# Performance work log

Hardware: AMD Instinct MI355X
Metric: run time of the kernel (lower is better)

## Reference

```python
import jax, jax.numpy as jnp
import numpy as np

K = 9  # 3x3 kernel taps

def conv2d(x, w, b):
    # stride 1, padding 1, NCHW / OIHW
    out = jax.lax.conv_general_dilated(x, w, (1, 1), ((1, 1), (1, 1)),
                                       dimension_numbers=('NCHW', 'OIHW', 'NCHW'))
    return out + b[None, :, None, None]

def deform_conv2d(x, offset, mask, w, b):
    # torchvision modulated deformable conv, kernel 3x3, stride 1, pad 1, dilation 1
    B, C, H, W = x.shape
    off = offset.reshape(B, K, 2, H, W)  # per-tap (dy, dx)
    ii = (jnp.arange(K) // 3).astype(x.dtype) - 1.0  # kernel row offset (pad=1)
    jj = (jnp.arange(K) % 3).astype(x.dtype) - 1.0   # kernel col offset
    hh = jnp.arange(H, dtype=x.dtype)[None, None, :, None]
    ww = jnp.arange(W, dtype=x.dtype)[None, None, None, :]
    py = hh + ii[None, :, None, None] + off[:, :, 0]  # [B,K,H,W] sample rows
    px = ww + jj[None, :, None, None] + off[:, :, 1]  # [B,K,H,W] sample cols

    y0 = jnp.floor(py); x0 = jnp.floor(px)
    dy = py - y0; dx = px - x0
    y0 = y0.astype(jnp.int32); x0 = x0.astype(jnp.int32)

    xf = x.reshape(B, C, H * W)

    def gather(yi, xi):
        valid = ((yi >= 0) & (yi < H) & (xi >= 0) & (xi < W)).astype(x.dtype)
        yc = jnp.clip(yi, 0, H - 1)
        xc = jnp.clip(xi, 0, W - 1)
        idx = (yc * W + xc).reshape(B, K * H * W)
        v = jax.vmap(lambda xb, ib: xb[:, ib])(xf, idx)  # [B,C,K*H*W]
        return v.reshape(B, C, K, H, W) * valid[:, None]

    v00 = gather(y0,     x0)
    v01 = gather(y0,     x0 + 1)
    v10 = gather(y0 + 1, x0)
    v11 = gather(y0 + 1, x0 + 1)

    dy = dy[:, None]; dx = dx[:, None]  # broadcast over channel dim
    val = (v00 * (1 - dy) * (1 - dx) + v01 * (1 - dy) * dx
           + v10 * dy * (1 - dx) + v11 * dy * dx)
    val = val * mask[:, None]  # sigmoid modulation, [B,1,K,H,W]

    out = jnp.einsum('ock,bckhw->bohw', w.reshape(w.shape[0], C, K), val)
    return out + b[None, :, None, None]

def setup_inputs() -> dict:
    key = jax.random.key(0)
    k1, k2, k3 = jax.random.split(key, 3)
    x = jax.random.normal(k1, (8, 3, 512, 512), dtype=jnp.float32)
    w_off = jax.random.normal(k2, (27, 3, 3, 3), dtype=jnp.float32) * 0.05
    b_off = jnp.zeros((27,), dtype=jnp.float32)
    w_def = jax.random.normal(k3, (3, 3, 3, 3), dtype=jnp.float32) * 0.1
    b_def = jnp.zeros((3,), dtype=jnp.float32)
    return {'x': x, 'w_off': w_off, 'b_off': b_off, 'w_def': w_def, 'b_def': b_def}

def reference(x, w_off, b_off, w_def, b_def):
    ow = conv2d(x, w_off, b_off)            # [B,27,H,W]
    offset = ow[:, :18]                      # 2*9 offsets
    mask = jax.nn.sigmoid(ow[:, 18:])        # 9 modulation masks
    return deform_conv2d(x, offset, mask, w_def, b_def)
```

## Files before the change

### kernel.cpp

```cpp
#include <hip/hip_runtime.h>
#include <math.h>

typedef float f2 __attribute__((ext_vector_type(2)));
typedef float f2u __attribute__((ext_vector_type(2), aligned(4)));
typedef float f4 __attribute__((ext_vector_type(4)));

#define BN 8
#define CIN 3
#define HH 512
#define WW 512
#define KK 9
#define PATCH 27
#define TAPBLK 96

__global__ void reorder_weights(const float* __restrict__ w_off,
                                const float* __restrict__ w_def,
                                float* __restrict__ ws)
{
    for (int idx = threadIdx.x; idx < KK * TAPBLK; idx += blockDim.x) {
        const int k = idx / TAPBLK;
        const int r = idx % TAPBLK;
        float v = 0.0f;
        if (r < 56) {
            const int q = r >> 1, half = r & 1;
            if (q < PATCH) v = w_off[(2 * k + half) * PATCH + q];
        } else if (r < 84) {
            const int i = r - 56;
            if (i < PATCH) v = w_off[(18 + k) * PATCH + i];
        } else {
            const int j = r - 84;
            const int c = j >> 2, o = j & 3;
            if (o < 3) v = w_def[o * PATCH + c * KK + k];
        }
        ws[idx] = v;
    }
}

__global__ __launch_bounds__(256) void deform_fused_kernel(
    const float* __restrict__ x,
    const float* __restrict__ wsw,
    const float* __restrict__ b_off,
    const float* __restrict__ b_def,
    float* __restrict__ out)
{
    const int w = blockIdx.x * blockDim.x + threadIdx.x;
    const int h = blockIdx.y;
    const int b = blockIdx.z;

    const size_t plane = (size_t)HH * WW;
    const float* xb = x + (size_t)b * CIN * plane;

    float patch[28];
    patch[27] = 0.0f;
    #pragma unroll
    for (int c = 0; c < CIN; ++c) {
        const float* xp = xb + c * plane;
        #pragma unroll
        for (int t = 0; t < KK; ++t) {
            const int yy = h + t / 3 - 1;
            const int xx = w + t % 3 - 1;
            const bool in = (yy >= 0) & (yy < HH) & (xx >= 0) & (xx < WW);
            patch[c * KK + t] = in ? xp[yy * WW + xx] : 0.0f;
        }
    }

    f2 acc01 = { b_def[0], b_def[1] };
    float acc2 = b_def[2];

    #pragma unroll 1
    for (int k = 0; k < KK; ++k) {
        const float* blk = wsw + k * TAPBLK;

        f2 oyx = { b_off[2 * k], b_off[2 * k + 1] };
        float om = b_off[18 + k];

        #pragma unroll
        for (int j = 0; j < 14; ++j) {
            const f4 wq = *(const f4*)(blk + 4 * j);
            const float p0 = patch[2 * j];
            const float p1 = patch[2 * j + 1];
            const f2 w0 = { wq.x, wq.y };
            const f2 w1 = { wq.z, wq.w };
            const f2 pp0 = { p0, p0 };
            const f2 pp1 = { p1, p1 };
            oyx = __builtin_elementwise_fma(w0, pp0, oyx);
            oyx = __builtin_elementwise_fma(w1, pp1, oyx);
        }
        #pragma unroll
        for (int j = 0; j < 7; ++j) {
            const f4 wm4 = *(const f4*)(blk + 56 + 4 * j);
            om = fmaf(wm4.x, patch[4 * j],     om);
            om = fmaf(wm4.y, patch[4 * j + 1], om);
            om = fmaf(wm4.z, patch[4 * j + 2], om);
            om = fmaf(wm4.w, patch[4 * j + 3], om);
        }

        const float m = 1.0f / (1.0f + __expf(-om));

        const float py = (float)h + (float)(k / 3 - 1) + oyx.x;
        const float px = (float)w + (float)(k % 3 - 1) + oyx.y;
        const float y0f = floorf(py);
        const float x0f = floorf(px);
        const float dy = py - y0f;
        const float dx = px - x0f;
        const int y0 = (int)y0f;
        const int x0 = (int)x0f;

        const f2 dxp = { 1.0f - dx, dx };
        const f2 wT = dxp * (1.0f - dy);
        const f2 wB = dxp * dy;

        const int interior = (y0 >= 0) & (y0 + 1 < HH) & (x0 >= 0) & (x0 + 1 < WW);

        if (__all(interior)) {
            const int idx = y0 * WW + x0;
            #pragma unroll
            for (int c = 0; c < CIN; ++c) {
                const float* xp = xb + c * plane + idx;
                const f2 vT = *(const f2u*)(xp);
                const f2 vB = *(const f2u*)(xp + WW);
                f2 s = vT * wT;
                s = __builtin_elementwise_fma(vB, wB, s);
                const float val = (s.x + s.y) * m;
                const f4 wq = *(const f4*)(blk + 84 + 4 * c);
                const f2 w01 = { wq.x, wq.y };
                const f2 vv = { val, val };
                acc01 = __builtin_elementwise_fma(w01, vv, acc01);
                acc2 = fmaf(wq.z, val, acc2);
            }
        } else {
            const bool vy0 = (y0 >= 0)     & (y0 < HH);
            const bool vy1 = (y0 + 1 >= 0) & (y0 + 1 < HH);
            const bool vx0 = (x0 >= 0)     & (x0 < WW);
            const bool vx1 = (x0 + 1 >= 0) & (x0 + 1 < WW);

            const int yc0 = min(max(y0, 0), HH - 1);
            const int yc1 = min(max(y0 + 1, 0), HH - 1);
            const int xc0 = min(max(x0, 0), WW - 1);
            const int xc1 = min(max(x0 + 1, 0), WW - 1);

            #pragma unroll
            for (int c = 0; c < CIN; ++c) {
                const float* xp = xb + c * plane;
                const float v00 = (vy0 & vx0) ? xp[yc0 * WW + xc0] : 0.0f;
                const float v01 = (vy0 & vx1) ? xp[yc0 * WW + xc1] : 0.0f;
                const float v10 = (vy1 & vx0) ? xp[yc1 * WW + xc0] : 0.0f;
                const float v11 = (vy1 & vx1) ? xp[yc1 * WW + xc1] : 0.0f;

                const float val =
                    (v00 * wT.x + v01 * wT.y + v10 * wB.x + v11 * wB.y) * m;
                const f4 wq = *(const f4*)(blk + 84 + 4 * c);
                const f2 w01 = { wq.x, wq.y };
                const f2 vv = { val, val };
                acc01 = __builtin_elementwise_fma(w01, vv, acc01);
                acc2 = fmaf(wq.z, val, acc2);
            }
        }
    }

    const size_t base = (size_t)b * (CIN * plane) + (size_t)h * WW + w;
    out[base]             = acc01.x;
    out[base + plane]     = acc01.y;
    out[base + 2 * plane] = acc2;
}

extern "C" void kernel_launch(void* const* d_in, const int* in_sizes, int n_in,
                              void* d_out, int out_size, void* d_ws, size_t ws_size,
                              hipStream_t stream) {
    const float* x     = (const float*)d_in[0];
    const float* w_off = (const float*)d_in[1];
    const float* b_off = (const float*)d_in[2];
    const float* w_def = (const float*)d_in[3];
    const float* b_def = (const float*)d_in[4];
    float* out = (float*)d_out;
    float* wsw = (float*)d_ws;

    reorder_weights<<<1, 256, 0, stream>>>(w_off, w_def, wsw);

    dim3 block(256, 1, 1);
    dim3 grid(WW / 256, HH, BN);
    deform_fused_kernel<<<grid, block, 0, stream>>>(x, wsw, b_off, b_def, out);
}
```

Measured before the change: 183.7 us.

## Compute all offset-conv channels upfront with packed FMAs and unroll tap loop

Reorders the offset-conv weights into patch-major rows of 28 packed channels so all 27 offset/mask channels are computed in one pass of packed f2 FMAs before the tap loop. The mask channels, previously done with scalar FMAs, now also use packed math, and the offset biases are folded into the workspace. The tap loop is fully unrolled because the per-tap values now live in registers. This raises register pressure (14 f2 accumulators plus the patch) and may lower occupancy.

Measured after the change: 460.6 us. 2.51x slower.

```diff
diff --git a/kernel.cpp b/kernel.cpp
--- a/kernel.cpp
+++ b/kernel.cpp
@@ -11,26 +11,32 @@
 #define WW 512
 #define KK 9
 #define PATCH 27
-#define TAPBLK 96
+
+
+__device__ __forceinline__ int pair_ch(int q) {
+    const int p = q >> 1, hh = q & 1;
+    return (p < 9) ? (2 * p + hh) : (18 + 2 * (p - 9) + hh);
+}
 
 __global__ void reorder_weights(const float* __restrict__ w_off,
                                 const float* __restrict__ w_def,
+                                const float* __restrict__ b_off,
                                 float* __restrict__ ws)
 {
-    for (int idx = threadIdx.x; idx < KK * TAPBLK; idx += blockDim.x) {
-        const int k = idx / TAPBLK;
-        const int r = idx % TAPBLK;
+    for (int idx = threadIdx.x; idx < 908; idx += blockDim.x) {
         float v = 0.0f;
-        if (r < 56) {
-            const int q = r >> 1, half = r & 1;
-            if (q < PATCH) v = w_off[(2 * k + half) * PATCH + q];
-        } else if (r < 84) {
-            const int i = r - 56;
-            if (i < PATCH) v = w_off[(18 + k) * PATCH + i];
-        } else {
-            const int j = r - 84;
-            const int c = j >> 2, o = j & 3;
+        if (idx < 756) {
+            const int j = idx / 28, q = idx % 28;
+            const int ch = pair_ch(q);
+            if (ch < PATCH) v = w_off[ch * PATCH + j];
+        } else if (idx >= 768 && idx < 876) {
+            const int r = idx - 768;
+            const int k = r / 12, c = (r % 12) >> 2, o = r & 3;
             if (o < 3) v = w_def[o * PATCH + c * KK + k];
+        } else if (idx >= 880) {
+            const int q = idx - 880;
+            const int ch = pair_ch(q);
+            if (ch < PATCH) v = b_off[ch];
         }
         ws[idx] = v;
     }
@@ -39,7 +45,6 @@
 __global__ __launch_bounds__(256) void deform_fused_kernel(
     const float* __restrict__ x,
     const float* __restrict__ wsw,
-    const float* __restrict__ b_off,
     const float* __restrict__ b_def,
     float* __restrict__ out)
 {
@@ -50,8 +55,7 @@
     const size_t plane = (size_t)HH * WW;
     const float* xb = x + (size_t)b * CIN * plane;
 
-    float patch[28];
-    patch[27] = 0.0f;
+    float patch[PATCH];
     #pragma unroll
     for (int c = 0; c < CIN; ++c) {
         const float* xp = xb + c * plane;
@@ -64,37 +68,28 @@
         }
     }
 
+    f2 cv[14];
+    #pragma unroll
+    for (int p = 0; p < 14; ++p) cv[p] = *(const f2*)(wsw + 880 + 2 * p);
+
+    #pragma unroll
+    for (int j = 0; j < PATCH; ++j) {
+        const f2 pp = { patch[j], patch[j] };
+        const float* row = wsw + j * 28;
+        #pragma unroll
+        for (int p = 0; p < 14; ++p) {
+            cv[p] = __builtin_elementwise_fma(*(const f2*)(row + 2 * p), pp, cv[p]);
+        }
+    }
+
     f2 acc01 = { b_def[0], b_def[1] };
     float acc2 = b_def[2];
 
-    #pragma unroll 1
+    #pragma unroll
     for (int k = 0; k < KK; ++k) {
-        const float* blk = wsw + k * TAPBLK;
-
-        f2 oyx = { b_off[2 * k], b_off[2 * k + 1] };
-        float om = b_off[18 + k];
-
-        #pragma unroll
-        for (int j = 0; j < 14; ++j) {
-            const f4 wq = *(const f4*)(blk + 4 * j);
-            const float p0 = patch[2 * j];
-            const float p1 = patch[2 * j + 1];
-            const f2 w0 = { wq.x, wq.y };
-            const f2 w1 = { wq.z, wq.w };
-            const f2 pp0 = { p0, p0 };
-            const f2 pp1 = { p1, p1 };
-            oyx = __builtin_elementwise_fma(w0, pp0, oyx);
-            oyx = __builtin_elementwise_fma(w1, pp1, oyx);
-        }
-        #pragma unroll
-        for (int j = 0; j < 7; ++j) {
-            const f4 wm4 = *(const f4*)(blk + 56 + 4 * j);
-            om = fmaf(wm4.x, patch[4 * j],     om);
-            om = fmaf(wm4.y, patch[4 * j + 1], om);
-            om = fmaf(wm4.z, patch[4 * j + 2], om);
-            om = fmaf(wm4.w, patch[4 * j + 3], om);
-        }
-
+        const f2 oyx = cv[k];
+        const float om = (k & 1) ? cv[9 + (k >> 1)].y
+                                 : cv[9 + (k >> 1)].x;
         const float m = 1.0f / (1.0f + __expf(-om));
 
         const float py = (float)h + (float)(k / 3 - 1) + oyx.x;
@@ -111,6 +106,7 @@
         const f2 wB = dxp * dy;
 
         const int interior = (y0 >= 0) & (y0 + 1 < HH) & (x0 >= 0) & (x0 + 1 < WW);
+        const float* blkc = wsw + 768 + k * 12;
 
         if (__all(interior)) {
             const int idx = y0 * WW + x0;
@@ -122,7 +118,7 @@
                 f2 s = vT * wT;
                 s = __builtin_elementwise_fma(vB, wB, s);
                 const float val = (s.x + s.y) * m;
-                const f4 wq = *(const f4*)(blk + 84 + 4 * c);
+                const f4 wq = *(const f4*)(blkc + 4 * c);
                 const f2 w01 = { wq.x, wq.y };
                 const f2 vv = { val, val };
                 acc01 = __builtin_elementwise_fma(w01, vv, acc01);
@@ -149,7 +145,7 @@
 
                 const float val =
                     (v00 * wT.x + v01 * wT.y + v10 * wB.x + v11 * wB.y) * m;
-                const f4 wq = *(const f4*)(blk + 84 + 4 * c);
+                const f4 wq = *(const f4*)(blkc + 4 * c);
                 const f2 w01 = { wq.x, wq.y };
                 const f2 vv = { val, val };
                 acc01 = __builtin_elementwise_fma(w01, vv, acc01);
@@ -175,9 +171,9 @@
     float* out = (float*)d_out;
     float* wsw = (float*)d_ws;
 
-    reorder_weights<<<1, 256, 0, stream>>>(w_off, w_def, wsw);
+    reorder_weights<<<1, 256, 0, stream>>>(w_off, w_def, b_off, wsw);
 
     dim3 block(256, 1, 1);
     dim3 grid(WW / 256, HH, BN);
-    deform_fused_kernel<<<grid, block, 0, stream>>>(x, wsw, b_off, b_def, out);
+    deform_fused_kernel<<<grid, block, 0, stream>>>(x, wsw, b_def, out);
 }
```

## Software-pipeline tap loop to overlap bilinear gathers with next tap's offset compute

Applied to the files above, without the earlier changes.

The tap loop is restructured so each iteration first issues the gather loads for the current tap, then computes the next tap's offsets and mask from the patch, and only afterwards consumes the gathered values. The aim is to hide global-memory gather latency behind the offset-convolution FMAs. The cost is more live registers (six f2 gather values plus next-tap state), which may reduce occupancy.

Measured after the change: 182.4 us. Within noise of the previous version (-0.7%).

```diff
diff --git a/kernel.cpp b/kernel.cpp
--- a/kernel.cpp
+++ b/kernel.cpp
@@ -64,16 +64,18 @@
         }
     }
 
+    const float hf = (float)h;
+    const float wf = (float)w;
+
     f2 acc01 = { b_def[0], b_def[1] };
     float acc2 = b_def[2];
 
-    #pragma unroll 1
-    for (int k = 0; k < KK; ++k) {
-        const float* blk = wsw + k * TAPBLK;
-
-        f2 oyx = { b_off[2 * k], b_off[2 * k + 1] };
-        float om = b_off[18 + k];
-
+    f2 oyx;
+    float om;
+    {
+        const float* blk = wsw;
+        f2 a = { b_off[0], b_off[1] };
+        float s = b_off[18];
         #pragma unroll
         for (int j = 0; j < 14; ++j) {
             const f4 wq = *(const f4*)(blk + 4 * j);
@@ -83,22 +85,34 @@
             const f2 w1 = { wq.z, wq.w };
             const f2 pp0 = { p0, p0 };
             const f2 pp1 = { p1, p1 };
-            oyx = __builtin_elementwise_fma(w0, pp0, oyx);
-            oyx = __builtin_elementwise_fma(w1, pp1, oyx);
+            a = __builtin_elementwise_fma(w0, pp0, a);
+            a = __builtin_elementwise_fma(w1, pp1, a);
         }
         #pragma unroll
         for (int j = 0; j < 7; ++j) {
             const f4 wm4 = *(const f4*)(blk + 56 + 4 * j);
-            om = fmaf(wm4.x, patch[4 * j],     om);
-            om = fmaf(wm4.y, patch[4 * j + 1], om);
-            om = fmaf(wm4.z, patch[4 * j + 2], om);
-            om = fmaf(wm4.w, patch[4 * j + 3], om);
-        }
+            s = fmaf(wm4.x, patch[4 * j],     s);
+            s = fmaf(wm4.y, patch[4 * j + 1], s);
+            s = fmaf(wm4.z, patch[4 * j + 2], s);
+            s = fmaf(wm4.w, patch[4 * j + 3], s);
+        }
+        oyx = a;
+        om = s;
+    }
+
+    #pragma unroll 1
+    for (int k = 1; k <= KK; ++k) {
+        const int kp = k - 1;
+        const float* blkp = wsw + kp * TAPBLK;
+
+        const f4 cw0 = *(const f4*)(blkp + 84);
+        const f4 cw1 = *(const f4*)(blkp + 88);
+        const f4 cw2 = *(const f4*)(blkp + 92);
 
         const float m = 1.0f / (1.0f + __expf(-om));
 
-        const float py = (float)h + (float)(k / 3 - 1) + oyx.x;
-        const float px = (float)w + (float)(k % 3 - 1) + oyx.y;
+        const float py = hf + (float)(kp / 3 - 1) + oyx.x;
+        const float px = wf + (float)(kp % 3 - 1) + oyx.y;
         const float y0f = floorf(py);
         const float x0f = floorf(px);
         const float dy = py - y0f;
@@ -112,22 +126,15 @@
 
         const int interior = (y0 >= 0) & (y0 + 1 < HH) & (x0 >= 0) & (x0 + 1 < WW);
 
+        f2 vT0, vB0, vT1, vB1, vT2, vB2;
         if (__all(interior)) {
             const int idx = y0 * WW + x0;
-            #pragma unroll
-            for (int c = 0; c < CIN; ++c) {
-                const float* xp = xb + c * plane + idx;
-                const f2 vT = *(const f2u*)(xp);
-                const f2 vB = *(const f2u*)(xp + WW);
-                f2 s = vT * wT;
-                s = __builtin_elementwise_fma(vB, wB, s);
-                const float val = (s.x + s.y) * m;
-                const f4 wq = *(const f4*)(blk + 84 + 4 * c);
-                const f2 w01 = { wq.x, wq.y };
-                const f2 vv = { val, val };
-                acc01 = __builtin_elementwise_fma(w01, vv, acc01);
-                acc2 = fmaf(wq.z, val, acc2);
-            }
+            const float* xp0 = xb + idx;
+            const float* xp1 = xp0 + plane;
+            const float* xp2 = xp1 + plane;
+            vT0 = *(const f2u*)(xp0);  vB0 = *(const f2u*)(xp0 + WW);
+            vT1 = *(const f2u*)(xp1);  vB1 = *(const f2u*)(xp1 + WW);
+            vT2 = *(const f2u*)(xp2);  vB2 = *(const f2u*)(xp2 + WW);
         } else {
             const bool vy0 = (y0 >= 0)     & (y0 < HH);
             const bool vy1 = (y0 + 1 >= 0) & (y0 + 1 < HH);
@@ -139,22 +146,75 @@
             const int xc0 = min(max(x0, 0), WW - 1);
             const int xc1 = min(max(x0 + 1, 0), WW - 1);
 
+            const float* xp0 = xb;
+            const float* xp1 = xp0 + plane;
+            const float* xp2 = xp1 + plane;
+
+            vT0.x = (vy0 & vx0) ? xp0[yc0 * WW + xc0] : 0.0f;
+            vT0.y = (vy0 & vx1) ? xp0[yc0 * WW + xc1] : 0.0f;
+            vB0.x = (vy1 & vx0) ? xp0[yc1 * WW + xc0] : 0.0f;
+            vB0.y = (vy1 & vx1) ? xp0[yc1 * WW + xc1] : 0.0f;
+            vT1.x = (vy0 & vx0) ? xp1[yc0 * WW + xc0] : 0.0f;
+            vT1.y = (vy0 & vx1) ? xp1[yc0 * WW + xc1] : 0.0f;
+            vB1.x = (vy1 & vx0) ? xp1[yc1 * WW + xc0] : 0.0f;
+            vB1.y = (vy1 & vx1) ? xp1[yc1 * WW + xc1] : 0.0f;
+            vT2.x = (vy0 & vx0) ? xp2[yc0 * WW + xc0] : 0.0f;
+            vT2.y = (vy0 & vx1) ? xp2[yc0 * WW + xc1] : 0.0f;
+            vB2.x = (vy1 & vx0) ? xp2[yc1 * WW + xc0] : 0.0f;
+            vB2.y = (vy1 & vx1) ? xp2[yc1 * WW + xc1] : 0.0f;
+        }
+
+        if (k < KK) {
+            const float* blk = wsw + k * TAPBLK;
+            f2 a = { b_off[2 * k], b_off[2 * k + 1] };
+            float s = b_off[18 + k];
             #pragma unroll
-            for (int c = 0; c < CIN; ++c) {
-                const float* xp = xb + c * plane;
-                const float v00 = (vy0 & vx0) ? xp[yc0 * WW + xc0] : 0.0f;
-                const float v01 = (vy0 & vx1) ? xp[yc0 * WW + xc1] : 0.0f;
-                const float v10 = (vy1 & vx0) ? xp[yc1 * WW + xc0] : 0.0f;
-                const float v11 = (vy1 & vx1) ? xp[yc1 * WW + xc1] : 0.0f;
-
-                const float val =
-                    (v00 * wT.x + v01 * wT.y + v10 * wB.x + v11 * wB.y) * m;
-                const f4 wq = *(const f4*)(blk + 84 + 4 * c);
-                const f2 w01 = { wq.x, wq.y };
-                const f2 vv = { val, val };
-                acc01 = __builtin_elementwise_fma(w01, vv, acc01);
-                acc2 = fmaf(wq.z, val, acc2);
+            for (int j = 0; j < 14; ++j) {
+                const f4 wq = *(const f4*)(blk + 4 * j);
+                const float p0 = patch[2 * j];
+                const float p1 = patch[2 * j + 1];
+                const f2 w0 = { wq.x, wq.y };
+                const f2 w1 = { wq.z, wq.w };
+                const f2 pp0 = { p0, p0 };
+                const f2 pp1 = { p1, p1 };
+                a = __builtin_elementwise_fma(w0, pp0, a);
+                a = __builtin_elementwise_fma(w1, pp1, a);
             }
+            #pragma unroll
+            for (int j = 0; j < 7; ++j) {
+                const f4 wm4 = *(const f4*)(blk + 56 + 4 * j);
+                s = fmaf(wm4.x, patch[4 * j],     s);
+                s = fmaf(wm4.y, patch[4 * j + 1], s);
+                s = fmaf(wm4.z, patch[4 * j + 2], s);
+                s = fmaf(wm4.w, patch[4 * j + 3], s);
+            }
+            oyx = a;
+            om = s;
+        }
+
+        {
+            f2 s0 = vT0 * wT;
+            s0 = __builtin_elementwise_fma(vB0, wB, s0);
+            const float val0 = (s0.x + s0.y) * m;
+            f2 s1 = vT1 * wT;
+            s1 = __builtin_elementwise_fma(vB1, wB, s1);
+            const float val1 = (s1.x + s1.y) * m;
+            f2 s2 = vT2 * wT;
+            s2 = __builtin_elementwise_fma(vB2, wB, s2);
+            const float val2 = (s2.x + s2.y) * m;
+
+            const f2 w01_0 = { cw0.x, cw0.y };
+            const f2 w01_1 = { cw1.x, cw1.y };
+            const f2 w01_2 = { cw2.x, cw2.y };
+            const f2 vv0 = { val0, val0 };
+            const f2 vv1 = { val1, val1 };
+            const f2 vv2 = { val2, val2 };
+            acc01 = __builtin_elementwise_fma(w01_0, vv0, acc01);
+            acc2 = fmaf(cw0.z, val0, acc2);
+            acc01 = __builtin_elementwise_fma(w01_1, vv1, acc01);
+            acc2 = fmaf(cw1.z, val1, acc2);
+            acc01 = __builtin_elementwise_fma(w01_2, vv2, acc01);
+            acc2 = fmaf(cw2.z, val2, acc2);
         }
     }
 
```

## Compute two pixels per thread and software-pipeline offset conv with gathers

Applied to the files above, without the earlier changes.

Each thread now handles two adjacent output pixels, sharing the input patch rows and the weight loads between them. The loop is software-pipelined: the offset/mask convolution for the next tap is computed while the bilinear gathers for the current tap are in flight. Gathers for all three channels are issued up front, and outputs are written as vector stores. The grid is halved, which lowers the thread count and raises register pressure. That could reduce occupancy and latency hiding.

Measured after the change: 211.1 us. 14.9% more time.

```diff
diff --git a/kernel.cpp b/kernel.cpp
--- a/kernel.cpp
+++ b/kernel.cpp
@@ -36,6 +36,43 @@
     }
 }
 
+#define PAT(J, P) ((J) >= PATCH ? 0.0f : pr[((J) / 9) * 3 + (((J) % 9) / 3)][((J) % 3) + (P)])
+
+#define CONV_TAP(K) do {                                                \
+    const float* blk_ = wsw + (K) * TAPBLK;                             \
+    f2 aA_ = { b_off[2 * (K)], b_off[2 * (K) + 1] };                    \
+    f2 aB_ = aA_;                                                       \
+    float sA_ = b_off[18 + (K)];                                        \
+    float sB_ = sA_;                                                    \
+    _Pragma("unroll")                                                   \
+    for (int j = 0; j < 14; ++j) {                                      \
+        const f4 wq_ = *(const f4*)(blk_ + 4 * j);                      \
+        const f2 wv0_ = { wq_.x, wq_.y };                               \
+        const f2 wv1_ = { wq_.z, wq_.w };                               \
+        const f2 pA0_ = { PAT(2 * j, 0),     PAT(2 * j, 0) };           \
+        const f2 pB0_ = { PAT(2 * j, 1),     PAT(2 * j, 1) };           \
+        const f2 pA1_ = { PAT(2 * j + 1, 0), PAT(2 * j + 1, 0) };       \
+        const f2 pB1_ = { PAT(2 * j + 1, 1), PAT(2 * j + 1, 1) };       \
+        aA_ = __builtin_elementwise_fma(wv0_, pA0_, aA_);               \
+        aB_ = __builtin_elementwise_fma(wv0_, pB0_, aB_);               \
+        aA_ = __builtin_elementwise_fma(wv1_, pA1_, aA_);               \
+        aB_ = __builtin_elementwise_fma(wv1_, pB1_, aB_);               \
+    }                                                                   \
+    _Pragma("unroll")                                                   \
+    for (int j = 0; j < 7; ++j) {                                       \
+        const f4 wm_ = *(const f4*)(blk_ + 56 + 4 * j);                 \
+        sA_ = fmaf(wm_.x, PAT(4 * j, 0),     sA_);                      \
+        sB_ = fmaf(wm_.x, PAT(4 * j, 1),     sB_);                      \
+        sA_ = fmaf(wm_.y, PAT(4 * j + 1, 0), sA_);                      \
+        sB_ = fmaf(wm_.y, PAT(4 * j + 1, 1), sB_);                      \
+        sA_ = fmaf(wm_.z, PAT(4 * j + 2, 0), sA_);                      \
+        sB_ = fmaf(wm_.z, PAT(4 * j + 2, 1), sB_);                      \
+        sA_ = fmaf(wm_.w, PAT(4 * j + 3, 0), sA_);                      \
+        sB_ = fmaf(wm_.w, PAT(4 * j + 3, 1), sB_);                      \
+    }                                                                   \
+    oyxA = aA_; omA = sA_; oyxB = aB_; omB = sB_;                       \
+} while (0)
+
 __global__ __launch_bounds__(256) void deform_fused_kernel(
     const float* __restrict__ x,
     const float* __restrict__ wsw,
@@ -43,125 +80,203 @@
     const float* __restrict__ b_def,
     float* __restrict__ out)
 {
-    const int w = blockIdx.x * blockDim.x + threadIdx.x;
+    const int t = threadIdx.x;
+    const int w0 = 2 * t;
     const int h = blockIdx.y;
     const int b = blockIdx.z;
 
     const size_t plane = (size_t)HH * WW;
     const float* xb = x + (size_t)b * CIN * plane;
 
-    float patch[28];
-    patch[27] = 0.0f;
+    float pr[9][4];
     #pragma unroll
     for (int c = 0; c < CIN; ++c) {
         const float* xp = xb + c * plane;
         #pragma unroll
-        for (int t = 0; t < KK; ++t) {
-            const int yy = h + t / 3 - 1;
-            const int xx = w + t % 3 - 1;
-            const bool in = (yy >= 0) & (yy < HH) & (xx >= 0) & (xx < WW);
-            patch[c * KK + t] = in ? xp[yy * WW + xx] : 0.0f;
+        for (int r = 0; r < 3; ++r) {
+            const int yy = h + r - 1;
+            if (yy >= 0 && yy < HH) {
+                const float* rowp = xp + yy * WW;
+                const f2 mid = *(const f2u*)(rowp + w0);
+                pr[c * 3 + r][1] = mid.x;
+                pr[c * 3 + r][2] = mid.y;
+                pr[c * 3 + r][0] = (t > 0)   ? rowp[w0 - 1] : 0.0f;
+                pr[c * 3 + r][3] = (t < 255) ? rowp[w0 + 2] : 0.0f;
+            } else {
+                pr[c * 3 + r][0] = 0.0f;
+                pr[c * 3 + r][1] = 0.0f;
+                pr[c * 3 + r][2] = 0.0f;
+                pr[c * 3 + r][3] = 0.0f;
+            }
         }
     }
 
-    f2 acc01 = { b_def[0], b_def[1] };
-    float acc2 = b_def[2];
+    const float hf = (float)h;
+    const float wfA = (float)w0;
+    const float wfB = (float)(w0 + 1);
+
+    f2 accA01 = { b_def[0], b_def[1] };
+    float accA2 = b_def[2];
+    f2 accB01 = accA01;
+    float accB2 = accA2;
+
+    f2 oyxA, oyxB;
+    float omA, omB;
+    CONV_TAP(0);
 
     #pragma unroll 1
-    for (int k = 0; k < KK; ++k) {
-        const float* blk = wsw + k * TAPBLK;
-
-        f2 oyx = { b_off[2 * k], b_off[2 * k + 1] };
-        float om = b_off[18 + k];
-
-        #pragma unroll
-        for (int j = 0; j < 14; ++j) {
-            const f4 wq = *(const f4*)(blk + 4 * j);
-            const float p0 = patch[2 * j];
-            const float p1 = patch[2 * j + 1];
-            const f2 w0 = { wq.x, wq.y };
-            const f2 w1 = { wq.z, wq.w };
-            const f2 pp0 = { p0, p0 };
-            const f2 pp1 = { p1, p1 };
-            oyx = __builtin_elementwise_fma(w0, pp0, oyx);
-            oyx = __builtin_elementwise_fma(w1, pp1, oyx);
-        }
-        #pragma unroll
-        for (int j = 0; j < 7; ++j) {
-            const f4 wm4 = *(const f4*)(blk + 56 + 4 * j);
-            om = fmaf(wm4.x, patch[4 * j],     om);
-            om = fmaf(wm4.y, patch[4 * j + 1], om);
-            om = fmaf(wm4.z, patch[4 * j + 2], om);
-            om = fmaf(wm4.w, patch[4 * j + 3], om);
-        }
-
-        const float m = 1.0f / (1.0f + __expf(-om));
-
-        const float py = (float)h + (float)(k / 3 - 1) + oyx.x;
-        const float px = (float)w + (float)(k % 3 - 1) + oyx.y;
-        const float y0f = floorf(py);
-        const float x0f = floorf(px);
-        const float dy = py - y0f;
-        const float dx = px - x0f;
-        const int y0 = (int)y0f;
-        const int x0 = (int)x0f;
-
-        const f2 dxp = { 1.0f - dx, dx };
-        const f2 wT = dxp * (1.0f - dy);
-        const f2 wB = dxp * dy;
-
-        const int interior = (y0 >= 0) & (y0 + 1 < HH) & (x0 >= 0) & (x0 + 1 < WW);
-
-        if (__all(interior)) {
-            const int idx = y0 * WW + x0;
-            #pragma unroll
-            for (int c = 0; c < CIN; ++c) {
-                const float* xp = xb + c * plane + idx;
-                const f2 vT = *(const f2u*)(xp);
-                const f2 vB = *(const f2u*)(xp + WW);
-                f2 s = vT * wT;
-                s = __builtin_elementwise_fma(vB, wB, s);
-                const float val = (s.x + s.y) * m;
-                const f4 wq = *(const f4*)(blk + 84 + 4 * c);
-                const f2 w01 = { wq.x, wq.y };
-                const f2 vv = { val, val };
-                acc01 = __builtin_elementwise_fma(w01, vv, acc01);
-                acc2 = fmaf(wq.z, val, acc2);
+    for (int k = 1; k <= KK; ++k) {
+        const int kp = k - 1;
+        const float* blkp = wsw + kp * TAPBLK;
+
+        const f4 cw0 = *(const f4*)(blkp + 84);
+        const f4 cw1 = *(const f4*)(blkp + 88);
+        const f4 cw2 = *(const f4*)(blkp + 92);
+
+        const float mA = 1.0f / (1.0f + __expf(-omA));
+        const float mB = 1.0f / (1.0f + __expf(-omB));
+
+        const float dyk = (float)(kp / 3 - 1);
+        const float dxk = (float)(kp % 3 - 1);
+
+        const float pyA = hf + dyk + oyxA.x;
+        const float pxA = wfA + dxk + oyxA.y;
+        const float pyB = hf + dyk + oyxB.x;
+        const float pxB = wfB + dxk + oyxB.y;
+
+        const float y0fA = floorf(pyA), x0fA = floorf(pxA);
+        const float y0fB = floorf(pyB), x0fB = floorf(pxB);
+        const float dyA = pyA - y0fA, dxA = pxA - x0fA;
+        const float dyB = pyB - y0fB, dxB = pxB - x0fB;
+        const int y0A = (int)y0fA, x0A = (int)x0fA;
+        const int y0B = (int)y0fB, x0B = (int)x0fB;
+
+        const f2 dxpA = { 1.0f - dxA, dxA };
+        const f2 wTA = dxpA * (1.0f - dyA);
+        const f2 wBA = dxpA * dyA;
+        const f2 dxpB = { 1.0f - dxB, dxB };
+        const f2 wTB = dxpB * (1.0f - dyB);
+        const f2 wBB = dxpB * dyB;
+
+        const int intA = (y0A >= 0) & (y0A + 1 < HH) & (x0A >= 0) & (x0A + 1 < WW);
+        const int intB = (y0B >= 0) & (y0B + 1 < HH) & (x0B >= 0) & (x0B + 1 < WW);
+
+        f2 vT0A, vB0A, vT1A, vB1A, vT2A, vB2A;
+        f2 vT0B, vB0B, vT1B, vB1B, vT2B, vB2B;
+
+        if (__all(intA & intB)) {
+            const int idxA = y0A * WW + x0A;
+            const int idxB = y0B * WW + x0B;
+            const float* p0A = xb + idxA;
+            const float* p0B = xb + idxB;
+            vT0A = *(const f2u*)(p0A);           vB0A = *(const f2u*)(p0A + WW);
+            vT0B = *(const f2u*)(p0B);           vB0B = *(const f2u*)(p0B + WW);
+            vT1A = *(const f2u*)(p0A + plane);   vB1A = *(const f2u*)(p0A + plane + WW);
+            vT1B = *(const f2u*)(p0B + plane);   vB1B = *(const f2u*)(p0B + plane + WW);
+            vT2A = *(const f2u*)(p0A + 2*plane); vB2A = *(const f2u*)(p0A + 2*plane + WW);
+            vT2B = *(const f2u*)(p0B + 2*plane); vB2B = *(const f2u*)(p0B + 2*plane + WW);
+        } else {
+            {
+                const bool vy0 = (y0A >= 0)     & (y0A < HH);
+                const bool vy1 = (y0A + 1 >= 0) & (y0A + 1 < HH);
+                const bool vx0 = (x0A >= 0)     & (x0A < WW);
+                const bool vx1 = (x0A + 1 >= 0) & (x0A + 1 < WW);
+                const int yc0 = min(max(y0A, 0), HH - 1);
+                const int yc1 = min(max(y0A + 1, 0), HH - 1);
+                const int xc0 = min(max(x0A, 0), WW - 1);
+                const int xc1 = min(max(x0A + 1, 0), WW - 1);
+                const float* p0 = xb;
+                const float* p1 = p0 + plane;
+                const float* p2 = p1 + plane;
+                vT0A.x = (vy0 & vx0) ? p0[yc0 * WW + xc0] : 0.0f;
+                vT0A.y = (vy0 & vx1) ? p0[yc0 * WW + xc1] : 0.0f;
+                vB0A.x = (vy1 & vx0) ? p0[yc1 * WW + xc0] : 0.0f;
+                vB0A.y = (vy1 & vx1) ? p0[yc1 * WW + xc1] : 0.0f;
+                vT1A.x = (vy0 & vx0) ? p1[yc0 * WW + xc0] : 0.0f;
+                vT1A.y = (vy0 & vx1) ? p1[yc0 * WW + xc1] : 0.0f;
+                vB1A.x = (vy1 & vx0) ? p1[yc1 * WW + xc0] : 0.0f;
+                vB1A.y = (vy1 & vx1) ? p1[yc1 * WW + xc1] : 0.0f;
+                vT2A.x = (vy0 & vx0) ? p2[yc0 * WW + xc0] : 0.0f;
+                vT2A.y = (vy0 & vx1) ? p2[yc0 * WW + xc1] : 0.0f;
+                vB2A.x = (vy1 & vx0) ? p2[yc1 * WW + xc0] : 0.0f;
+                vB2A.y = (vy1 & vx1) ? p2[yc1 * WW + xc1] : 0.0f;
             }
-        } else {
-            const bool vy0 = (y0 >= 0)     & (y0 < HH);
-            const bool vy1 = (y0 + 1 >= 0) & (y0 + 1 < HH);
-            const bool vx0 = (x0 >= 0)     & (x0 < WW);
-            const bool vx1 = (x0 + 1 >= 0) & (x0 + 1 < WW);
-
-            const int yc0 = min(max(y0, 0), HH - 1);
-            const int yc1 = min(max(y0 + 1, 0), HH - 1);
-            const int xc0 = min(max(x0, 0), WW - 1);
-            const int xc1 = min(max(x0 + 1, 0), WW - 1);
-
-            #pragma unroll
-            for (int c = 0; c < CIN; ++c) {
-                const float* xp = xb + c * plane;
-                const float v00 = (vy0 & vx0) ? xp[yc0 * WW + xc0] : 0.0f;
-                const float v01 = (vy0 & vx1) ? xp[yc0 * WW + xc1] : 0.0f;
-                const float v10 = (vy1 & vx0) ? xp[yc1 * WW + xc0] : 0.0f;
-                const float v11 = (vy1 & vx1) ? xp[yc1 * WW + xc1] : 0.0f;
-
-                const float val =
-                    (v00 * wT.x + v01 * wT.y + v10 * wB.x + v11 * wB.y) * m;
-                const f4 wq = *(const f4*)(blk + 84 + 4 * c);
-                const f2 w01 = { wq.x, wq.y };
-                const f2 vv = { val, val };
-                acc01 = __builtin_elementwise_fma(w01, vv, acc01);
-                acc2 = fmaf(wq.z, val, acc2);
+            {
+                const bool vy0 = (y0B >= 0)     & (y0B < HH);
+                const bool vy1 = (y0B + 1 >= 0) & (y0B + 1 < HH);
+                const bool vx0 = (x0B >= 0)     & (x0B < WW);
+                const bool vx1 = (x0B + 1 >= 0) & (x0B + 1 < WW);
+                const int yc0 = min(max(y0B, 0), HH - 1);
+                const int yc1 = min(max(y0B + 1, 0), HH - 1);
+                const int xc0 = min(max(x0B, 0), WW - 1);
+                const int xc1 = min(max(x0B + 1, 0), WW - 1);
+                const float* p0 = xb;
+                const float* p1 = p0 + plane;
+                const float* p2 = p1 + plane;
+                vT0B.x = (vy0 & vx0) ? p0[yc0 * WW + xc0] : 0.0f;
+                vT0B.y = (vy0 & vx1) ? p0[yc0 * WW + xc1] : 0.0f;
+                vB0B.x = (vy1 & vx0) ? p0[yc1 * WW + xc0] : 0.0f;
+                vB0B.y = (vy1 & vx1) ? p0[yc1 * WW + xc1] : 0.0f;
+                vT1B.x = (vy0 & vx0) ? p1[yc0 * WW + xc0] : 0.0f;
+                vT1B.y = (vy0 & vx1) ? p1[yc0 * WW + xc1] : 0.0f;
+                vB1B.x = (vy1 & vx0) ? p1[yc1 * WW + xc0] : 0.0f;
+                vB1B.y = (vy1 & vx1) ? p1[yc1 * WW + xc1] : 0.0f;
+                vT2B.x = (vy0 & vx0) ? p2[yc0 * WW + xc0] : 0.0f;
+                vT2B.y = (vy0 & vx1) ? p2[yc0 * WW + xc1] : 0.0f;
+                vB2B.x = (vy1 & vx0) ? p2[yc1 * WW + xc0] : 0.0f;
+                vB2B.y = (vy1 & vx1) ? p2[yc1 * WW + xc1] : 0.0f;
             }
         }
+
+        if (k < KK) {
+            CONV_TAP(k);
+        }
+
+        {
+            f2 s0 = vT0A * wTA; s0 = __builtin_elementwise_fma(vB0A, wBA, s0);
+            const float val0A = (s0.x + s0.y) * mA;
+            f2 s1 = vT1A * wTA; s1 = __builtin_elementwise_fma(vB1A, wBA, s1);
+            const float val1A = (s1.x + s1.y) * mA;
+            f2 s2 = vT2A * wTA; s2 = __builtin_elementwise_fma(vB2A, wBA, s2);
+            const float val2A = (s2.x + s2.y) * mA;
+
+            f2 u0 = vT0B * wTB; u0 = __builtin_elementwise_fma(vB0B, wBB, u0);
+            const float val0B = (u0.x + u0.y) * mB;
+            f2 u1 = vT1B * wTB; u1 = __builtin_elementwise_fma(vB1B, wBB, u1);
+            const float val1B = (u1.x + u1.y) * mB;
+            f2 u2 = vT2B * wTB; u2 = __builtin_elementwise_fma(vB2B, wBB, u2);
+            const float val2B = (u2.x + u2.y) * mB;
+
+            const f2 w01_0 = { cw0.x, cw0.y };
+            const f2 w01_1 = { cw1.x, cw1.y };
+            const f2 w01_2 = { cw2.x, cw2.y };
+
+            const f2 vv0A = { val0A, val0A };
+            const f2 vv1A = { val1A, val1A };
+            const f2 vv2A = { val2A, val2A };
+            accA01 = __builtin_elementwise_fma(w01_0, vv0A, accA01);
+            accA2 = fmaf(cw0.z, val0A, accA2);
+            accA01 = __builtin_elementwise_fma(w01_1, vv1A, accA01);
+            accA2 = fmaf(cw1.z, val1A, accA2);
+            accA01 = __builtin_elementwise_fma(w01_2, vv2A, accA01);
+            accA2 = fmaf(cw2.z, val2A, accA2);
+
+            const f2 vv0B = { val0B, val0B };
+            const f2 vv1B = { val1B, val1B };
+            const f2 vv2B = { val2B, val2B };
+            accB01 = __builtin_elementwise_fma(w01_0, vv0B, accB01);
+            accB2 = fmaf(cw0.z, val0B, accB2);
+            accB01 = __builtin_elementwise_fma(w01_1, vv1B, accB01);
+            accB2 = fmaf(cw1.z, val1B, accB2);
+            accB01 = __builtin_elementwise_fma(w01_2, vv2B, accB01);
+            accB2 = fmaf(cw2.z, val2B, accB2);
+        }
     }
 
-    const size_t base = (size_t)b * (CIN * plane) + (size_t)h * WW + w;
-    out[base]             = acc01.x;
-    out[base + plane]     = acc01.y;
-    out[base + 2 * plane] = acc2;
+    float* op = out + (size_t)b * (CIN * plane) + (size_t)h * WW + w0;
+    *(f2u*)(op)             = (f2){ accA01.x, accB01.x };
+    *(f2u*)(op + plane)     = (f2){ accA01.y, accB01.y };
+    *(f2u*)(op + 2 * plane) = (f2){ accA2,    accB2    };
 }
 
 extern "C" void kernel_launch(void* const* d_in, const int* in_sizes, int n_in,
@@ -178,6 +293,6 @@
     reorder_weights<<<1, 256, 0, stream>>>(w_off, w_def, wsw);
 
     dim3 block(256, 1, 1);
-    dim3 grid(WW / 256, HH, BN);
+    dim3 grid(1, HH, BN);
     deform_fused_kernel<<<grid, block, 0, stream>>>(x, wsw, b_off, b_def, out);
 }
```
